# Optimization experiments

Measured on AMD Instinct MI355X. Metric: run time of the kernel, lower is better.

Reference implementation:

```python
import jax, jax.numpy as jnp
import numpy as np

B, L, IN, H, E = 64, 255, 32, 256, 128
PAD = (L - 1) // 2
DN = ('NCH', 'OIH', 'NCH')


def setup_inputs() -> dict:
    ks = jax.random.split(jax.random.key(0), 10)
    r = lambda k, shp, s=0.05: jax.random.normal(k, shp, dtype=jnp.float32) * s
    return {
        's': jax.random.normal(ks[0], (B, L, IN), dtype=jnp.float32),
        'conv1_w': r(ks[1], (H, IN, L)),
        'conv1_b': r(ks[2], (H,)),
        'bn_gamma': jnp.ones((H,), jnp.float32),
        'bn_beta': jnp.zeros((H,), jnp.float32),
        'conv2_w': r(ks[3], (E, H, L)),
        'conv2_b': r(ks[4], (E,)),
        'pw1': r(ks[5], (E, H, L)),   # stacked Linear(L, H) weights, one per channel
        'pb1': r(ks[6], (E, H)),
        'pw2': r(ks[7], (E, 2, H)),   # stacked Linear(H, 2) weights
        'pb2': r(ks[8], (E, 2)),
    }


def reference(s, conv1_w, conv1_b, bn_gamma, bn_beta, conv2_w, conv2_b, pw1, pb1, pw2, pb2):
    x = jnp.transpose(s, (0, 2, 1))  # (B, IN, T)
    h = jax.lax.conv_general_dilated(x, conv1_w, (1,), [(PAD, PAD)], dimension_numbers=DN)
    h = jax.nn.relu(h + conv1_b[None, :, None])
    # BatchNorm1d in training mode: biased batch stats over (N, T)
    mean = h.mean(axis=(0, 2), keepdims=True)
    var = ((h - mean) ** 2).mean(axis=(0, 2), keepdims=True)
    h = (h - mean) * jax.lax.rsqrt(var + 1e-5) * bn_gamma[None, :, None] + bn_beta[None, :, None]
    z = jax.lax.conv_general_dilated(h, conv2_w, (1,), [(PAD, PAD)], dimension_numbers=DN)
    z = jnp.transpose(z + conv2_b[None, :, None], (0, 2, 1))  # (B, T, E)

    rf = jnp.fft.rfft(z, axis=1)                 # (B, F, E), F = L//2 + 1 == E
    power = jnp.abs(rf)[:, :, 1:] ** 2           # faithful channel-axis slice -> (B, F, E-1)
    freq_bins = jnp.fft.rfftfreq(L)[1:]          # (F-1,) == (E-1,)
    frequency = jnp.sum(freq_bins * power, axis=1) / jnp.sum(power, axis=1)  # (B, E-1)
    amplitude = 2.0 * jnp.sqrt(jnp.sum(power, axis=1)) / L                    # (B, E-1)
    offset = rf.real[:, :, 0] / L                                              # (B, E)

    # batched per-channel 2-layer MLP (replaces Python loop over embedding_dim)
    hmid = jax.nn.relu(jnp.einsum('btc,cht->bch', z, pw1) + pb1[None])  # (B, E, H)
    ang = jnp.einsum('bch,coh->bco', hmid, pw2) + pb2[None]             # (B, E, 2)
    phase = jnp.arctan2(ang[:, :, 1], ang[:, :, 0])                     # (B, E)
    return (amplitude, phase, frequency, offset)
```

## Files before the change

kernel.cpp:

```cpp
#include <hip/hip_runtime.h>
#include <math.h>

#define TB   64
#define TT   255
#define TIN  32
#define NH   256
#define NE   128
#define NK   255
#define NPAD 127

#define NF    384
#define NBINS 193
#define NFC   386
#define FCP   416
#define W2ROW 12288
#define HSROW 16384

typedef __attribute__((ext_vector_type(8))) short short8;
typedef __attribute__((ext_vector_type(4))) float float4v;

#define WSB_W2S  0u
#define WSB_Z    0u
#define WSB_HFU  8388608u
#define WSB_HMID 8388608u
#define WSB_ZSP  18972672u
#define WSB_HS   31621120u
#define WSB_BDH  56918144u
#define WSB_BDL  57115776u
#define WSB_BDM  57313408u
#define WSB_BWH  57511040u
#define WSB_BWL  57708672u
#define WSB_BWM  57906304u
#define WSB_D1   58103936u
#define WSB_BN   58105984u

#define O_AMP   0u
#define O_PHASE 8128u
#define O_FREQ  16320u
#define O_OFF   24448u

static __device__ __forceinline__ unsigned short f2bf(float f) {
  unsigned int u = __float_as_uint(f);
  unsigned int r = (u + 0x7FFFu + ((u >> 16) & 1u)) >> 16;
  return (unsigned short)r;
}
static __device__ __forceinline__ float bf2f(unsigned short s) {
  return __uint_as_float(((unsigned int)s) << 16);
}
static __device__ __forceinline__ short8 as_s8(uint4 v) {
  union { uint4 u; short8 s; } c; c.u = v; return c.s;
}

static __device__ __forceinline__ void split3(float x, unsigned short& h,
                                              unsigned short& l, unsigned short& m2) {
  h = f2bf(x);
  float r1 = x - bf2f(h);
  l = f2bf(r1);
  m2 = f2bf(r1 - bf2f(l));
}
static __device__ __forceinline__ void split_pack2(float x0, float x1,
    unsigned int& ph, unsigned int& pl, unsigned int& pm) {
  unsigned short h0, l0, m0_, h1, l1, m1_;
  split3(x0, h0, l0, m0_);
  split3(x1, h1, l1, m1_);
  ph = (unsigned int)h0 | ((unsigned int)h1 << 16);
  pl = (unsigned int)l0 | ((unsigned int)l1 << 16);
  pm = (unsigned int)m0_ | ((unsigned int)m1_ << 16);
}

static __device__ __forceinline__ void put_hi(unsigned int* __restrict__ U, int r,
                                              int p, unsigned int v) {
  const int sw = r & 7;
  U[r * 32 + ((((p >> 2) ^ sw) << 2) | (p & 3))] = v;
}
static __device__ __forceinline__ void put_lo(unsigned int* __restrict__ U, int r,
                                              int p, unsigned int v) {
  const int sw = r & 7;
  U[r * 32 + (((((p >> 2) + 4) ^ sw) << 2) | (p & 3))] = v;
}
static __device__ __forceinline__ void stage8_3(unsigned int* __restrict__ U,
                                                unsigned int* __restrict__ U2, int r,
                                                int p0, const float* __restrict__ v) {
#pragma unroll
  for (int q = 0; q < 4; ++q) {
    unsigned int ph, pl, pm;
    split_pack2(v[2 * q], v[2 * q + 1], ph, pl, pm);
    put_hi(U, r, p0 + q, ph);
    put_lo(U, r, p0 + q, pl);
    put_hi(U2, r, p0 + q, pm);
  }
}
static __device__ __forceinline__ void stage2_3(unsigned int* __restrict__ U,
                                                unsigned int* __restrict__ U2, int r,
                                                int p, float x0, float x1) {
  unsigned int ph, pl, pm;
  split_pack2(x0, x1, ph, pl, pm);
  put_hi(U, r, p, ph);
  put_lo(U, r, p, pl);
  put_hi(U2, r, p, pm);
}
static __device__ __forceinline__ short8 frag(const unsigned short* __restrict__ lds,
                                              int row, int quad, int part) {
  return *(const short8*)&lds[row * 64 + (((quad ^ (part << 2)) ^ (row & 7)) << 3)];
}
#define MF(a, b, c) __builtin_amdgcn_mfma_f32_16x16x32_bf16((a), (b), (c), 0, 0, 0)
#define MF6(accv, ahv, alv, a2v, bhv, blv, b2v) do {                              \
    accv = MF(ahv, bhv, accv);                                                    \
    accv = MF(ahv, blv, accv);                                                    \
    accv = MF(alv, bhv, accv);                                                    \
    accv = MF(alv, blv, accv);                                                    \
    accv = MF(ahv, b2v, accv);                                                    \
    accv = MF(a2v, bhv, accv);                                                    \
  } while (0)
#define MF5(accv, ahv, alv, a2v, bhv, blv) do {                                   \
    accv = MF(ahv, bhv, accv);                                                    \
    accv = MF(ahv, blv, accv);                                                    \
    accv = MF(alv, bhv, accv);                                                    \
    accv = MF(alv, blv, accv);                                                    \
    accv = MF(a2v, bhv, accv);                                                    \
  } while (0)

__global__ __launch_bounds__(256) void init_k(
    const float* __restrict__ w1, unsigned int* __restrict__ wp1u,
    unsigned int* __restrict__ bdh, unsigned int* __restrict__ bdl,
    unsigned int* __restrict__ bdm, unsigned int* __restrict__ bwh,
    unsigned int* __restrict__ bwl, unsigned int* __restrict__ bwm,
    float* __restrict__ d1, float* __restrict__ bn) {
  __shared__ float tile[512][33];
  const int bid = blockIdx.x, tid = threadIdx.x;
  if (bid == 0) {
    bn[tid] = 0.f;
    bn[256 + tid] = 0.f;
    return;
  }
  if (bid < 387) {
    float* sv = (float*)tile;
    const int m = bid - 1, t = tid;
    const int f = m >> 1, im = m & 1;
    const float C = 6.28318530717958647692f / 384.f;
    int r1 = (f * t) % 384;
    float th1 = C * (float)r1;
    sv[t] = (t == 255) ? 0.f : (im ? -sinf(th1) : cosf(th1));
    int a = f * (t - 127);
    int r2 = a % 384; if (r2 < 0) r2 += 384;
    float th2 = C * (float)r2;
    sv[256 + t] = (t == 255) ? 0.f : (im ? sinf(th2) : cosf(th2));
    __syncthreads();
    const int which = t >> 7, j = t & 127;
    unsigned int ph, pl, pm;
    split_pack2(sv[which * 256 + 2 * j], sv[which * 256 + 2 * j + 1], ph, pl, pm);
    size_t off = (size_t)m * 128 + j;
    if (which == 0) { bdh[off] = ph; bdl[off] = pl; bdm[off] = pm; }
    else            { bwh[off] = ph; bwl[off] = pl; bwm[off] = pm; }
    return;
  }
  if (bid < 389) {
    const int fc = (bid - 387) * 256 + tid;
    if (fc >= NFC) return;
    const int f = fc >> 1, im = fc & 1;
    const float C = 6.28318530717958647692f / 384.f;
    float s = 0.f;
    int r = 0;
    for (int t = 0; t < TT; ++t) {
      float th = C * (float)r;
      s += im ? -sinf(th) : cosf(th);
      r += f; if (r >= 384) r -= 384;
    }
    d1[fc] = s;
    return;
  }
  {
    const int q = bid - 389;
    const int et = q >> 3, kc = q & 7;
    const int kk0 = kc * 32, cnt = min(32, NK - kk0);
    for (int idx = tid; idx < 512 * 32; idx += 256) {
      int row = idx >> 5, kl = idx & 31;
      if (kl < cnt) {
        int e_l = row >> 5, i_l = row & 31;
        tile[row][kl] = w1[(size_t)((et * 16 + e_l) * TIN + i_l) * NK + kk0 + kl];
      }
    }
    __syncthreads();
    const int lane = tid >> 2, jp = (tid & 3) * 2;
    const int row0 = (lane & 15) * 32 + (lane >> 4) * 8 + jp;
    for (int kl = 0; kl < cnt; ++kl) {
      float w0 = tile[row0][kl], w1v = tile[row0 + 1][kl];
      unsigned short h0 = f2bf(w0), h1 = f2bf(w1v);
      unsigned short l0 = f2bf(w0 - bf2f(h0)), l1 = f2bf(w1v - bf2f(h1));
      size_t base = (size_t)(kk0 + kl) * 8192 + et * 512 + tid;
      wp1u[base] = (unsigned int)h0 | ((unsigned int)h1 << 16);
      wp1u[base + 256] = (unsigned int)l0 | ((unsigned int)l1 << 16);
    }
  }
}

#define C1_ROWS 384
__global__ __launch_bounds__(256, 2) void conv1_mfma(
    const float* __restrict__ s, const unsigned int* __restrict__ wp1u,
    const float* __restrict__ b1v, unsigned int* __restrict__ hfu,
    float* __restrict__ bn) {
  __shared__ __align__(16) unsigned short Alds[C1_ROWS * 64];
  const int th = blockIdx.x & 1, chg = blockIdx.x >> 1, b = blockIdx.y;
  const int tid = threadIdx.x, lane = tid & 63, wv = tid >> 6;
  const int quad = lane >> 4, l15 = lane & 15;
  const int tg = wv & 1, eg = wv >> 1;
  unsigned int* Au = (unsigned int*)Alds;

  for (int idx = tid; idx < C1_ROWS * 16; idx += 256) {
    int r = idx >> 4, p = idx & 15;
    int t = th * 128 + r - NPAD;
    float v0 = 0.f, v1 = 0.f;
    if (t >= 0 && t < TT) {
      const float* sp = &s[(size_t)(b * TT + t) * TIN + p * 2];
      v0 = sp[0]; v1 = sp[1];
    }
    unsigned short h0 = f2bf(v0), h1 = f2bf(v1);
    unsigned short l0 = f2bf(v0 - bf2f(h0)), l1 = f2bf(v1 - bf2f(h1));
    int sw = r & 7;
    Au[r * 32 + ((((p >> 2) ^ sw) << 2) | (p & 3))] = (unsigned int)h0 | ((unsigned int)h1 << 16);
    Au[r * 32 + (((((p >> 2) + 4) ^ sw) << 2) | (p & 3))] = (unsigned int)l0 | ((unsigned int)l1 << 16);
  }

#define LOADB1(buf, KK) do {                                                      \
    const uint4* _b = (const uint4*)(wp1u + (size_t)(KK) * 8192u) +               \
                      (chg * 4 + eg * 2) * 128;                                   \
    buf[0] = _b[lane];          buf[1] = _b[64 + lane];                           \
    buf[2] = _b[128 + lane];    buf[3] = _b[192 + lane];                          \
  } while (0)

#define MSTEP1(KK, buf) do {                                                      \
    short8 bh0 = as_s8(buf[0]), bl0 = as_s8(buf[1]);                              \
    short8 bh1 = as_s8(buf[2]), bl1 = as_s8(buf[3]);                              \
    _Pragma("unroll")                                                             \
    for (int mi = 0; mi < 4; ++mi) {                                              \
      const int row = tg * 64 + mi * 16 + l15 + (KK);                             \
      const int sw = row & 7;                                                     \
      short8 ah = *(const short8*)&Alds[row * 64 + ((quad ^ sw) << 3)];           \
      short8 al = *(const short8*)&Alds[row * 64 + (((quad ^ 4) ^ sw) << 3)];     \
      acc[mi][0] = MF(ah, bh0, acc[mi][0]);                                       \
      acc[mi][0] = MF(ah, bl0, acc[mi][0]);                                       \
      acc[mi][0] = MF(al, bh0, acc[mi][0]);                                       \
      acc[mi][1] = MF(ah, bh1, acc[mi][1]);                                       \
      acc[mi][1] = MF(ah, bl1, acc[mi][1]);                                       \
      acc[mi][1] = MF(al, bh1, acc[mi][1]);                                       \
    }                                                                             \
  } while (0)

  uint4 b0[4], b1x[4], b2x[4];
  LOADB1(b0, 0);
  LOADB1(b1x, 1);
  LOADB1(b2x, 2);
  __syncthreads();

  float4v acc[4][2];
#pragma unroll
  for (int mi = 0; mi < 4; ++mi)
#pragma unroll
    for (int ni = 0; ni < 2; ++ni) acc[mi][ni] = (float4v)(0.f);

  for (int kp = 0; kp < 84; ++kp) {
    const int kk = kp * 3;
    MSTEP1(kk, b0);     LOADB1(b0, kk + 3);
    MSTEP1(kk + 1, b1x); LOADB1(b1x, kk + 4);
    MSTEP1(kk + 2, b2x); LOADB1(b2x, kk + 5);
  }
  MSTEP1(252, b0);
  MSTEP1(253, b1x);
  MSTEP1(254, b2x);

  float s1[2] = {0.f, 0.f}, s2[2] = {0.f, 0.f};
#pragma unroll
  for (int mi = 0; mi < 4; ++mi) {
#pragma unroll
    for (int ni = 0; ni < 2; ++ni) {
      int ch = chg * 64 + (eg * 2 + ni) * 16 + l15;
      float bias = b1v[ch];
#pragma unroll
      for (int r = 0; r < 4; ++r) {
        int t = th * 128 + tg * 64 + mi * 16 + quad * 4 + r;
        if (t < TT) {
          float v = fmaxf(acc[mi][ni][r] + bias, 0.f);
          unsigned short vh = f2bf(v);
          unsigned short vl = f2bf(v - bf2f(vh));
          hfu[(size_t)(b * 256 + t) * NH + ch] =
              (unsigned int)vh | ((unsigned int)vl << 16);
          s1[ni] += v; s2[ni] += v * v;
        }
      }
    }
  }
#pragma unroll
  for (int ni = 0; ni < 2; ++ni) {
    s1[ni] += __shfl_xor(s1[ni], 16);
    s1[ni] += __shfl_xor(s1[ni], 32);
    s2[ni] += __shfl_xor(s2[ni], 16);
    s2[ni] += __shfl_xor(s2[ni], 32);
    if (quad == 0) {
      int ch = chg * 64 + (eg * 2 + ni) * 16 + l15;
      atomicAdd(&bn[ch], s1[ni]);
      atomicAdd(&bn[256 + ch], s2[ni]);
    }
  }
#undef LOADB1
#undef MSTEP1
}


#define LOAD_A_PLANES(PH, PL, PM) do {                                            \
    if (fcA < NFC) {                                                              \
      size_t ab = (size_t)fcA * 128 + (k0 >> 1) + hfA * 8;                        \
      uint4 h0v = *(const uint4*)(PH + ab), h1v = *(const uint4*)(PH + ab + 4);   \
      uint4 l0v = *(const uint4*)(PL + ab), l1v = *(const uint4*)(PL + ab + 4);   \
      uint4 m0v = *(const uint4*)(PM + ab), m1v = *(const uint4*)(PM + ab + 4);   \
      _Pragma("unroll")                                                           \
      for (int q = 0; q < 4; ++q) {                                               \
        put_hi(Au, rA, hfA * 8 + q, ((const unsigned int*)&h0v)[q]);              \
        put_hi(Au, rA, hfA * 8 + 4 + q, ((const unsigned int*)&h1v)[q]);          \
        put_lo(Au, rA, hfA * 8 + q, ((const unsigned int*)&l0v)[q]);              \
        put_lo(Au, rA, hfA * 8 + 4 + q, ((const unsigned int*)&l1v)[q]);          \
        put_hi(A2u, rA, hfA * 8 + q, ((const unsigned int*)&m0v)[q]);             \
        put_hi(A2u, rA, hfA * 8 + 4 + q, ((const unsigned int*)&m1v)[q]);         \
      }                                                                           \
    } else {                                                                      \
      _Pragma("unroll")                                                           \
      for (int q = 0; q < 8; ++q) {                                               \
        put_hi(Au, rA, hfA * 8 + q, 0u);                                          \
        put_lo(Au, rA, hfA * 8 + q, 0u);                                          \
        put_hi(A2u, rA, hfA * 8 + q, 0u);                                         \
      }                                                                           \
    }                                                                             \
  } while (0)

__global__ __launch_bounds__(256, 2) void dftH_mfma(
    const unsigned int* __restrict__ hfu, const float* __restrict__ bn,
    const float* __restrict__ gamma, const float* __restrict__ beta,
    const unsigned int* __restrict__ bdh, const unsigned int* __restrict__ bdl,
    const unsigned int* __restrict__ bdm, const float* __restrict__ d1,
    float* __restrict__ H) {
  __shared__ __align__(16) unsigned short Alds[128 * 64];
  __shared__ __align__(16) unsigned short A2lds[128 * 64];
  __shared__ __align__(16) unsigned short Blds[64 * 64];
  __shared__ float scs[64], shs[64];
  const int b = blockIdx.x, m0 = blockIdx.y * 128, h0c = blockIdx.z * 64;
  const int tid = threadIdx.x, lane = tid & 63, wv = tid >> 6;
  const int quad = lane >> 4, l15 = lane & 15;
  const int wm = wv >> 1, wn = wv & 1;
  const int hl = tid & 63, g = tid >> 6;
  unsigned int* Au = (unsigned int*)Alds;
  unsigned int* A2u = (unsigned int*)A2lds;
  unsigned int* Bu = (unsigned int*)Blds;

  if (tid < 64) {
    int h = h0c + tid;
    const float inv = 1.0f / (TB * TT);
    float m = bn[h] * inv;
    float var = bn[256 + h] * inv - m * m;
    float sc = gamma[h] / sqrtf(var + 1e-5f);
    scs[tid] = sc;
    shs[tid] = beta[h] - m * sc;
  }

  float4v acc[4][2];
#pragma unroll
  for (int i = 0; i < 4; ++i)
#pragma unroll
    for (int j = 0; j < 2; ++j) acc[i][j] = (float4v)(0.f);

  const int rA = tid >> 1, hfA = tid & 1;
  const int fcA = m0 + rA;

  for (int kk = 0; kk < 8; ++kk) {
    const int k0 = kk * 32;
    if (kk) __syncthreads();
    LOAD_A_PLANES(bdh, bdl, bdm);
#pragma unroll
    for (int j = 0; j < 4; ++j) {
      int tp = g * 4 + j;
      int t0 = k0 + tp * 2;
      unsigned int u0 = (t0 < TT)
          ? hfu[(size_t)(b * 256 + t0) * NH + h0c + hl] : 0u;
      unsigned int u1 = (t0 + 1 < TT)
          ? hfu[(size_t)(b * 256 + t0 + 1) * NH + h0c + hl] : 0u;
      unsigned int hp = (u0 & 0xFFFFu) | ((u1 & 0xFFFFu) << 16);
      unsigned int lp = (u0 >> 16) | (u1 & 0xFFFF0000u);
      put_hi(Bu, hl, tp, hp);
      put_lo(Bu, hl, tp, lp);
    }
    __syncthreads();
    short8 bh[2], bl[2];
#pragma unroll
    for (int ni = 0; ni < 2; ++ni) {
      int rb = wn * 32 + ni * 16 + l15;
      bh[ni] = frag(Blds, rb, quad, 0);
      bl[ni] = frag(Blds, rb, quad, 1);
    }
#pragma unroll
    for (int mi = 0; mi < 4; ++mi) {
      int ra = wm * 64 + mi * 16 + l15;
      short8 ah = frag(Alds, ra, quad, 0);
      short8 al = frag(Alds, ra, quad, 1);
      short8 a2 = frag(A2lds, ra, quad, 0);
#pragma unroll
      for (int ni = 0; ni < 2; ++ni) MF5(acc[mi][ni], ah, al, a2, bh[ni], bl[ni]);
    }
  }
#pragma unroll
  for (int mi = 0; mi < 4; ++mi) {
    int fc0 = m0 + wm * 64 + mi * 16 + quad * 4;
#pragma unroll
    for (int ni = 0; ni < 2; ++ni) {
      int hli = wn * 32 + ni * 16 + l15;
      float scv = scs[hli];
      float shv = shs[hli];
#pragma unroll
      for (int r = 0; r < 4; ++r) {
        int fc = fc0 + r;
        if (fc < NFC)
          H[(size_t)fc * HSROW + b * 256 + h0c + hli] =
              scv * acc[mi][ni][r] + shv * d1[fc];
      }
    }
  }
}

__global__ __launch_bounds__(256, 2) void w2prep_mfma(
    const float* __restrict__ w2, const unsigned int* __restrict__ bwh,
    const unsigned int* __restrict__ bwl, const unsigned int* __restrict__ bwm,
    float* __restrict__ W, int h0c, int hcnt) {
  __shared__ __align__(16) unsigned short Alds[128 * 64];
  __shared__ __align__(16) unsigned short A2lds[128 * 64];
  __shared__ __align__(16) unsigned short Blds[128 * 64];
  __shared__ __align__(16) unsigned short B2lds[128 * 64];
  const int n0 = blockIdx.x * 128, m0 = blockIdx.y * 128;
  const int tid = threadIdx.x, lane = tid & 63, wv = tid >> 6;
  const int quad = lane >> 4, l15 = lane & 15;
  const int wm = wv >> 1, wn = wv & 1;
  unsigned int* Au = (unsigned int*)Alds;
  unsigned int* A2u = (unsigned int*)A2lds;
  unsigned int* Bu = (unsigned int*)Blds;
  unsigned int* B2u = (unsigned int*)B2lds;

  float4v acc[4][4];
#pragma unroll
  for (int i = 0; i < 4; ++i)
#pragma unroll
    for (int j = 0; j < 4; ++j) acc[i][j] = (float4v)(0.f);

  const int rA = tid >> 1, hfA = tid & 1;
  const int fcA = m0 + rA;
  const int lane8 = tid & 7, rsub = tid >> 3;

  for (int kk = 0; kk < 8; ++kk) {
    const int k0 = kk * 32;
    if (kk) __syncthreads();
    LOAD_A_PLANES(bwh, bwl, bwm);
#pragma unroll
    for (int pass = 0; pass < 4; ++pass) {
      int row = pass * 32 + rsub;
      int n = n0 + row;
      int e = n / 96, hl = n - e * 96;
      int ok = (hl < hcnt);
      const float* src = w2 + ((size_t)(e * NH + h0c + hl)) * NK;
      int kb = k0 + lane8 * 4;
      float f0 = (ok && kb < NK) ? src[kb] : 0.f;
      float f1 = (ok && kb + 1 < NK) ? src[kb + 1] : 0.f;
      float f2 = (ok && kb + 2 < NK) ? src[kb + 2] : 0.f;
      float f3 = (ok && kb + 3 < NK) ? src[kb + 3] : 0.f;
      stage2_3(Bu, B2u, row, lane8 * 2, f0, f1);
      stage2_3(Bu, B2u, row, lane8 * 2 + 1, f2, f3);
    }
    __syncthreads();
    short8 bh[4], bl[4], b2[4];
#pragma unroll
    for (int ni = 0; ni < 4; ++ni) {
      int rb = wn * 64 + ni * 16 + l15;
      bh[ni] = frag(Blds, rb, quad, 0);
      bl[ni] = frag(Blds, rb, quad, 1);
      b2[ni] = frag(B2lds, rb, quad, 0);
    }
#pragma unroll
    for (int mi = 0; mi < 4; ++mi) {
      int ra = wm * 64 + mi * 16 + l15;
      short8 ah = frag(Alds, ra, quad, 0);
      short8 al = frag(Alds, ra, quad, 1);
      short8 a2 = frag(A2lds, ra, quad, 0);
#pragma unroll
      for (int ni = 0; ni < 4; ++ni) MF6(acc[mi][ni], ah, al, a2, bh[ni], bl[ni], b2[ni]);
    }
  }
#pragma unroll
  for (int mi = 0; mi < 4; ++mi) {
    int fc0 = m0 + wm * 64 + mi * 16 + quad * 4;
#pragma unroll
    for (int ni = 0; ni < 4; ++ni) {
      int n = n0 + wn * 64 + ni * 16 + l15;
#pragma unroll
      for (int r = 0; r < 4; ++r) {
        if (fc0 + r < NFC) W[(size_t)(fc0 + r) * W2ROW + n] = acc[mi][ni][r];
      }
    }
  }
}

__global__ __launch_bounds__(256, 2) void fgemm_mfma(
    const float* __restrict__ H, const float* __restrict__ W,
    float* __restrict__ zsp, int c96, int nks, int first) {
  __shared__ __align__(16) unsigned short Alds[64 * 64];
  __shared__ __align__(16) unsigned short A2lds[64 * 64];
  __shared__ __align__(16) unsigned short Blds[128 * 64];
  __shared__ __align__(16) unsigned short B2lds[128 * 64];
  const int ri = blockIdx.x, f = blockIdx.y;
  const int tid = threadIdx.x, lane = tid & 63, wv = tid >> 6;
  const int quad = lane >> 4, l15 = lane & 15;
  const int wm = wv >> 1, wn = wv & 1;
  unsigned int* Au = (unsigned int*)Alds;
  unsigned int* A2u = (unsigned int*)A2lds;
  unsigned int* Bu = (unsigned int*)Blds;
  unsigned int* B2u = (unsigned int*)B2lds;

  float4v acc[2][4];
#pragma unroll
  for (int i = 0; i < 2; ++i)
#pragma unroll
    for (int j = 0; j < 4; ++j) acc[i][j] = (float4v)(0.f);

  const int rA = tid >> 2, qA = tid & 3;
  const int rB = tid >> 1, hB = tid & 1;

  for (int ph = 0; ph < 2 * nks; ++ph) {
    const int ca = (ph >= nks) ? 1 : 0;
    const int hsub = (ph - ca * nks) * 32;
    if (ph) __syncthreads();
    {
      float va[8];
      const float4* s4 = (const float4*)(H + (size_t)(2 * f + ca) * HSROW +
                                         rA * 256 + c96 + hsub + qA * 8);
      *(float4*)(va + 0) = s4[0]; *(float4*)(va + 4) = s4[1];
      stage8_3(Au, A2u, rA, qA * 4, va);
    }
    {
      const int cb = ri ^ ca;
      const int neg = (ri == 0 && ca == 1);
      float vb[16];
      const float4* s4 = (const float4*)(W + (size_t)(2 * f + cb) * W2ROW +
                                         rB * 96 + hsub + hB * 16);
      *(float4*)(vb + 0) = s4[0]; *(float4*)(vb + 4) = s4[1];
      *(float4*)(vb + 8) = s4[2]; *(float4*)(vb + 12) = s4[3];
      if (neg) {
#pragma unroll
        for (int q = 0; q < 16; ++q) vb[q] = -vb[q];
      }
      stage8_3(Bu, B2u, rB, hB * 8, vb);
      stage8_3(Bu, B2u, rB, hB * 8 + 4, vb + 8);
    }
    __syncthreads();
    short8 bh[4], bl[4], b2[4];
#pragma unroll
    for (int ni = 0; ni < 4; ++ni) {
      int rb = wn * 64 + ni * 16 + l15;
      bh[ni] = frag(Blds, rb, quad, 0);
      bl[ni] = frag(Blds, rb, quad, 1);
      b2[ni] = frag(B2lds, rb, quad, 0);
    }
#pragma unroll
    for (int mi = 0; mi < 2; ++mi) {
      int ra = wm * 32 + mi * 16 + l15;
      short8 ah = frag(Alds, ra, quad, 0);
      short8 al = frag(Alds, ra, quad, 1);
      short8 a2 = frag(A2lds, ra, quad, 0);
#pragma unroll
      for (int ni = 0; ni < 4; ++ni) MF6(acc[mi][ni], ah, al, a2, bh[ni], bl[ni], b2[ni]);
    }
  }
  float* Z = zsp + (size_t)(2 * f + ri) * 8192;
#pragma unroll
  for (int mi = 0; mi < 2; ++mi) {
#pragma unroll
    for (int ni = 0; ni < 4; ++ni) {
      int e = wn * 64 + ni * 16 + l15;
#pragma unroll
      for (int r = 0; r < 4; ++r) {
        int b = wm * 32 + mi * 16 + quad * 4 + r;
        size_t off = (size_t)b * 128 + e;
        if (first) Z[off] = acc[mi][ni][r];
        else       Z[off] += acc[mi][ni][r];
      }
    }
  }
}

__global__ __launch_bounds__(256, 2) void idft_mfma(
    const float* __restrict__ zsp, const unsigned int* __restrict__ bdh,
    const unsigned int* __restrict__ bdl, const unsigned int* __restrict__ bdm,
    const float* __restrict__ b2, float* __restrict__ z) {
  __shared__ __align__(16) unsigned short Alds[128 * 64];
  __shared__ __align__(16) unsigned short A2lds[128 * 64];
  __shared__ __align__(16) unsigned short Blds[64 * 64];
  __shared__ __align__(16) unsigned short B2lds[64 * 64];
  const int n0 = blockIdx.x * 64, m0 = blockIdx.y * 128;
  const int tid = threadIdx.x, lane = tid & 63, wv = tid >> 6;
  const int quad = lane >> 4, l15 = lane & 15;
  const int wm = wv >> 1, wn = wv & 1;
  const int tl = tid & 63, g = tid >> 6;
  unsigned int* Au = (unsigned int*)Alds;
  unsigned int* A2u = (unsigned int*)A2lds;
  unsigned int* Bu = (unsigned int*)Blds;
  unsigned int* B2u = (unsigned int*)B2lds;

  float4v acc[4][2];
#pragma unroll
  for (int i = 0; i < 4; ++i)
#pragma unroll
    for (int j = 0; j < 2; ++j) acc[i][j] = (float4v)(0.f);

  for (int kk = 0; kk < 13; ++kk) {
    const int k0 = kk * 32;
    if (kk) __syncthreads();
#pragma unroll
    for (int i = 0; i < 8; ++i) {
      int combo = i * 4 + g;
      int tp = combo >> 1, beh = combo & 1;
      int fc0 = k0 + tp * 2;
      int row = beh * 64 + lane;
      float v0 = (fc0 < NFC) ? zsp[(size_t)fc0 * 8192 + m0 + row] : 0.f;
      float v1 = (fc0 + 1 < NFC) ? zsp[(size_t)(fc0 + 1) * 8192 + m0 + row] : 0.f;
      stage2_3(Au, A2u, row, tp, v0, v1);
    }
#pragma unroll
    for (int j = 0; j < 4; ++j) {
      int tp = g * 4 + j;
      int fc0 = k0 + tp * 2;
      float x0 = 0.f, x1 = 0.f;
      if (fc0 < NFC) {
        int fq = fc0 >> 1;
        float sw = ((fq == 0 || fq == 192) ? 1.f : 2.f) * (1.f / 384.f);
        int t = n0 + tl;
        int pi = t >> 1, hs = (t & 1) * 16;
        size_t o0 = (size_t)fc0 * 128 + pi, o1 = o0 + 128;
        x0 = (bf2f((unsigned short)(bdh[o0] >> hs)) +
              bf2f((unsigned short)(bdl[o0] >> hs)) +
              bf2f((unsigned short)(bdm[o0] >> hs))) * sw;
        x1 = (bf2f((unsigned short)(bdh[o1] >> hs)) +
              bf2f((unsigned short)(bdl[o1] >> hs)) +
              bf2f((unsigned short)(bdm[o1] >> hs))) * sw;
      }
      stage2_3(Bu, B2u, tl, tp, x0, x1);
    }
    __syncthreads();
    short8 bh[2], bl[2], b2f[2];
#pragma unroll
    for (int ni = 0; ni < 2; ++ni) {
      int rb = wn * 32 + ni * 16 + l15;
      bh[ni] = frag(Blds, rb, quad, 0);
      bl[ni] = frag(Blds, rb, quad, 1);
      b2f[ni] = frag(B2lds, rb, quad, 0);
    }
#pragma unroll
    for (int mi = 0; mi < 4; ++mi) {
      int ra = wm * 64 + mi * 16 + l15;
      short8 ah = frag(Alds, ra, quad, 0);
      short8 al = frag(Alds, ra, quad, 1);
      short8 a2 = frag(A2lds, ra, quad, 0);
#pragma unroll
      for (int ni = 0; ni < 2; ++ni) MF6(acc[mi][ni], ah, al, a2, bh[ni], bl[ni], b2f[ni]);
    }
  }
#pragma unroll
  for (int mi = 0; mi < 4; ++mi) {
#pragma unroll
    for (int ni = 0; ni < 2; ++ni) {
      int t = n0 + wn * 32 + ni * 16 + l15;
#pragma unroll
      for (int r = 0; r < 4; ++r) {
        int be = m0 + wm * 64 + mi * 16 + quad * 4 + r;
        if (t < TT) z[(size_t)be * TT + t] = acc[mi][ni][r] + b2[be & 127];
      }
    }
  }
}

__global__ __launch_bounds__(256) void mlp1_k(const float* __restrict__ z,
                                              const float* __restrict__ pw1,
                                              const float* __restrict__ pb1,
                                              float* __restrict__ hmid) {
  const int TC = 128;
  __shared__ float zl[TC * 68];
  __shared__ float pl[TC * 68];
  const int c = blockIdx.y, h0 = blockIdx.x * 64, tid = threadIdx.x;
  const int h4 = tid & 15, b4 = tid >> 4;
  float acc[4][4];
#pragma unroll
  for (int a = 0; a < 4; ++a)
#pragma unroll
    for (int bb = 0; bb < 4; ++bb) acc[a][bb] = 0.f;
  for (int t0 = 0; t0 < TT; t0 += TC) {
    const int tc = min(TC, TT - t0);
    __syncthreads();
    for (int idx = tid; idx < 64 * tc; idx += 256) {
      int r = idx / tc, t = idx - r * tc;
      zl[t * 68 + r] = z[(size_t)(r * NE + c) * TT + t0 + t];
      pl[t * 68 + r] = pw1[(size_t)(c * NH + h0 + r) * TT + t0 + t];
    }
    __syncthreads();
    for (int t = 0; t < tc; ++t) {
      float4 zv = *(const float4*)&zl[t * 68 + b4 * 4];
      float4 pv = *(const float4*)&pl[t * 68 + h4 * 4];
      float zz[4] = {zv.x, zv.y, zv.z, zv.w};
      float pp[4] = {pv.x, pv.y, pv.z, pv.w};
#pragma unroll
      for (int a = 0; a < 4; ++a)
#pragma unroll
        for (int bb = 0; bb < 4; ++bb) acc[a][bb] = fmaf(pp[a], zz[bb], acc[a][bb]);
    }
  }
#pragma unroll
  for (int a = 0; a < 4; ++a) {
    int hh = h0 + h4 * 4 + a;
    float bias = pb1[c * NH + hh];
#pragma unroll
    for (int bb = 0; bb < 4; ++bb) {
      int bidx = b4 * 4 + bb;
      float v = acc[a][bb] + bias;
      hmid[(size_t)(bidx * NE + c) * NH + hh] = fmaxf(v, 0.f);
    }
  }
}

__global__ __launch_bounds__(256) void tail_k(const float* __restrict__ hmid,
                                              const float* __restrict__ pw2,
                                              const float* __restrict__ pb2,
                                              const float* __restrict__ z,
                                              float* __restrict__ out) {
  __shared__ float zr[TT];
  __shared__ float ct[TT];
  const int bid = blockIdx.x, tid = threadIdx.x;
  const int lane = tid & 63, wv = tid >> 6;
  if (bid < 2048) {
    const int p = bid * 4 + wv;
    const int b = p >> 7, c = p & 127;
    const float4 hv = *(const float4*)&hmid[(size_t)(b * NE + c) * NH + lane * 4];
    const float4 p0 = *(const float4*)&pw2[(size_t)(c * 2 + 0) * NH + lane * 4];
    const float4 p1 = *(const float4*)&pw2[(size_t)(c * 2 + 1) * NH + lane * 4];
    float s0 = hv.x * p0.x + hv.y * p0.y + hv.z * p0.z + hv.w * p0.w;
    float s1 = hv.x * p1.x + hv.y * p1.y + hv.z * p1.z + hv.w * p1.w;
#pragma unroll
    for (int off = 32; off; off >>= 1) {
      s0 += __shfl_down(s0, off);
      s1 += __shfl_down(s1, off);
    }
    if (lane == 0) {
      float a0 = s0 + pb2[c * 2 + 0];
      float a1 = s1 + pb2[c * 2 + 1];
      out[O_PHASE + b * NE + c] = atan2f(a1, a0);
    }
    return;
  }
  if (bid < 4096) {
    const int q = bid - 2048;
    const int b = q >> 5, c = (q & 31) * 4 + wv;
    const float* row = z + (size_t)(b * NE + c) * TT;
    float s1 = 0.f, s2 = 0.f;
    for (int idx = lane; idx < TT; idx += 64) {
      float v = row[idx];
      s1 += v; s2 += v * v;
    }
#pragma unroll
    for (int off = 32; off; off >>= 1) {
      s1 += __shfl_down(s1, off);
      s2 += __shfl_down(s2, off);
    }
    if (lane == 0 && c >= 1) {
      float P = 0.5f * (255.f * s2 + s1 * s1);
      out[O_AMP + b * 127 + (c - 1)] = 2.f * sqrtf(P) / 255.f;
      out[O_FREQ + b * 127 + (c - 1)] = (float)c / 255.f;
    }
    return;
  }
  {
    const int b = bid - 4096;
    for (int idx = tid; idx < TT; idx += 256) {
      zr[idx] = z[(size_t)(b * NE + 0) * TT + idx];
      ct[idx] = cosf(6.283185307179586f * (float)idx / 255.f);
    }
    __syncthreads();
    if (tid < 128) {
      const int f = tid;
      float s = 0.f;
      int m = 0;
      for (int t = 0; t < TT; ++t) {
        s += zr[t] * ct[m];
        m += f; if (m >= TT) m -= TT;
      }
      out[O_OFF + b * NE + f] = s / 255.f;
    }
  }
}

extern "C" void kernel_launch(void* const* d_in, const int* in_sizes, int n_in,
                              void* d_out, int out_size, void* d_ws, size_t ws_size,
                              hipStream_t stream) {
  (void)in_sizes; (void)n_in; (void)out_size; (void)ws_size;
  const float* s       = (const float*)d_in[0];
  const float* conv1_w = (const float*)d_in[1];
  const float* conv1_b = (const float*)d_in[2];
  const float* bn_g    = (const float*)d_in[3];
  const float* bn_b    = (const float*)d_in[4];
  const float* conv2_w = (const float*)d_in[5];
  const float* conv2_b = (const float*)d_in[6];
  const float* pw1     = (const float*)d_in[7];
  const float* pb1     = (const float*)d_in[8];
  const float* pw2     = (const float*)d_in[9];
  const float* pb2     = (const float*)d_in[10];
  float* out = (float*)d_out;
  char* ws   = (char*)d_ws;

  unsigned int* wp1u = (unsigned int*)(ws + WSB_W2S);
  float* z    = (float*)(ws + WSB_Z);
  unsigned int* hfu = (unsigned int*)(ws + WSB_HFU);
  float* hmid = (float*)(ws + WSB_HMID);
  float* W2s  = (float*)(ws + WSB_W2S);
  float* Hs   = (float*)(ws + WSB_HS);
  float* zsp  = (float*)(ws + WSB_ZSP);
  unsigned int* bdh = (unsigned int*)(ws + WSB_BDH);
  unsigned int* bdl = (unsigned int*)(ws + WSB_BDL);
  unsigned int* bdm = (unsigned int*)(ws + WSB_BDM);
  unsigned int* bwh = (unsigned int*)(ws + WSB_BWH);
  unsigned int* bwl = (unsigned int*)(ws + WSB_BWL);
  unsigned int* bwm = (unsigned int*)(ws + WSB_BWM);
  float* d1 = (float*)(ws + WSB_D1);
  float* bn = (float*)(ws + WSB_BN);

  init_k<<<517, 256, 0, stream>>>(conv1_w, wp1u, bdh, bdl, bdm, bwh, bwl, bwm, d1, bn);
  conv1_mfma<<<dim3(8, TB), 256, 0, stream>>>(s, wp1u, conv1_b, hfu, bn);
  dftH_mfma<<<dim3(64, 4, 4), 256, 0, stream>>>(hfu, bn, bn_g, bn_b,
                                                bdh, bdl, bdm, d1, Hs);
  const int h0cs[3] = {0, 96, 192};
  const int hcnts[3] = {96, 96, 64};
  const int nkss[3] = {3, 3, 2};
  for (int c = 0; c < 3; ++c) {
    w2prep_mfma<<<dim3(96, 4), 256, 0, stream>>>(conv2_w, bwh, bwl, bwm, W2s,
                                                 h0cs[c], hcnts[c]);
    fgemm_mfma<<<dim3(2, NBINS), 256, 0, stream>>>(Hs, W2s, zsp,
                                                   h0cs[c], nkss[c], c == 0 ? 1 : 0);
  }
  idft_mfma<<<dim3(4, 64), 256, 0, stream>>>(zsp, bdh, bdl, bdm, conv2_b, z);
  mlp1_k<<<dim3(4, NE), 256, 0, stream>>>(z, pw1, pb1, hmid);
  tail_k<<<4160, 256, 0, stream>>>(hmid, pw2, pb2, z, out);
}
```

Baseline: 628.3 us.

## Compute conv1 via frequency-domain DFT GEMMs instead of direct MFMA convolution

Replaces the direct time-domain conv1 MFMA kernel (with bf16 hi/lo weight prepacking) with a spectral pipeline. Input and conv1 weights are transformed by DFT GEMMs, multiplied per frequency bin as complex GEMMs, then inverse-transformed with bias, ReLU and BN statistic accumulation fused in. This mirrors the approach already used for conv2 and cuts the O(L) per-output tap work. In exchange it adds two extra kernel launches, larger fp32 intermediates in workspace, and 3-way bf16 split arithmetic whose accuracy may differ from the previous 2-way split.

```diff
diff --git a/kernel.cpp b/kernel.cpp
--- a/kernel.cpp
+++ b/kernel.cpp
@@ -12,18 +12,20 @@
 #define NF    384
 #define NBINS 193
 #define NFC   386
-#define FCP   416
 #define W2ROW 12288
 #define HSROW 16384
 
 typedef __attribute__((ext_vector_type(8))) short short8;
 typedef __attribute__((ext_vector_type(4))) float float4v;
 
+#define WSB_SSP  0u
 #define WSB_W2S  0u
 #define WSB_Z    0u
+#define WSB_W1SP 4194304u
 #define WSB_HFU  8388608u
 #define WSB_HMID 8388608u
 #define WSB_ZSP  18972672u
+#define WSB_C1SP 25165824u
 #define WSB_HS   31621120u
 #define WSB_BDH  56918144u
 #define WSB_BDL  57115776u
@@ -46,9 +48,6 @@
 }
 static __device__ __forceinline__ float bf2f(unsigned short s) {
   return __uint_as_float(((unsigned int)s) << 16);
-}
-static __device__ __forceinline__ short8 as_s8(uint4 v) {
-  union { uint4 u; short8 s; } c; c.u = v; return c.s;
 }
 
 static __device__ __forceinline__ void split3(float x, unsigned short& h,
@@ -119,192 +118,6 @@
     accv = MF(alv, blv, accv);                                                    \
     accv = MF(a2v, bhv, accv);                                                    \
   } while (0)
-
-__global__ __launch_bounds__(256) void init_k(
-    const float* __restrict__ w1, unsigned int* __restrict__ wp1u,
-    unsigned int* __restrict__ bdh, unsigned int* __restrict__ bdl,
-    unsigned int* __restrict__ bdm, unsigned int* __restrict__ bwh,
-    unsigned int* __restrict__ bwl, unsigned int* __restrict__ bwm,
-    float* __restrict__ d1, float* __restrict__ bn) {
-  __shared__ float tile[512][33];
-  const int bid = blockIdx.x, tid = threadIdx.x;
-  if (bid == 0) {
-    bn[tid] = 0.f;
-    bn[256 + tid] = 0.f;
-    return;
-  }
-  if (bid < 387) {
-    float* sv = (float*)tile;
-    const int m = bid - 1, t = tid;
-    const int f = m >> 1, im = m & 1;
-    const float C = 6.28318530717958647692f / 384.f;
-    int r1 = (f * t) % 384;
-    float th1 = C * (float)r1;
-    sv[t] = (t == 255) ? 0.f : (im ? -sinf(th1) : cosf(th1));
-    int a = f * (t - 127);
-    int r2 = a % 384; if (r2 < 0) r2 += 384;
-    float th2 = C * (float)r2;
-    sv[256 + t] = (t == 255) ? 0.f : (im ? sinf(th2) : cosf(th2));
-    __syncthreads();
-    const int which = t >> 7, j = t & 127;
-    unsigned int ph, pl, pm;
-    split_pack2(sv[which * 256 + 2 * j], sv[which * 256 + 2 * j + 1], ph, pl, pm);
-    size_t off = (size_t)m * 128 + j;
-    if (which == 0) { bdh[off] = ph; bdl[off] = pl; bdm[off] = pm; }
-    else            { bwh[off] = ph; bwl[off] = pl; bwm[off] = pm; }
-    return;
-  }
-  if (bid < 389) {
-    const int fc = (bid - 387) * 256 + tid;
-    if (fc >= NFC) return;
-    const int f = fc >> 1, im = fc & 1;
-    const float C = 6.28318530717958647692f / 384.f;
-    float s = 0.f;
-    int r = 0;
-    for (int t = 0; t < TT; ++t) {
-      float th = C * (float)r;
-      s += im ? -sinf(th) : cosf(th);
-      r += f; if (r >= 384) r -= 384;
-    }
-    d1[fc] = s;
-    return;
-  }
-  {
-    const int q = bid - 389;
-    const int et = q >> 3, kc = q & 7;
-    const int kk0 = kc * 32, cnt = min(32, NK - kk0);
-    for (int idx = tid; idx < 512 * 32; idx += 256) {
-      int row = idx >> 5, kl = idx & 31;
-      if (kl < cnt) {
-        int e_l = row >> 5, i_l = row & 31;
-        tile[row][kl] = w1[(size_t)((et * 16 + e_l) * TIN + i_l) * NK + kk0 + kl];
-      }
-    }
-    __syncthreads();
-    const int lane = tid >> 2, jp = (tid & 3) * 2;
-    const int row0 = (lane & 15) * 32 + (lane >> 4) * 8 + jp;
-    for (int kl = 0; kl < cnt; ++kl) {
-      float w0 = tile[row0][kl], w1v = tile[row0 + 1][kl];
-      unsigned short h0 = f2bf(w0), h1 = f2bf(w1v);
-      unsigned short l0 = f2bf(w0 - bf2f(h0)), l1 = f2bf(w1v - bf2f(h1));
-      size_t base = (size_t)(kk0 + kl) * 8192 + et * 512 + tid;
-      wp1u[base] = (unsigned int)h0 | ((unsigned int)h1 << 16);
-      wp1u[base + 256] = (unsigned int)l0 | ((unsigned int)l1 << 16);
-    }
-  }
-}
-
-#define C1_ROWS 384
-__global__ __launch_bounds__(256, 2) void conv1_mfma(
-    const float* __restrict__ s, const unsigned int* __restrict__ wp1u,
-    const float* __restrict__ b1v, unsigned int* __restrict__ hfu,
-    float* __restrict__ bn) {
-  __shared__ __align__(16) unsigned short Alds[C1_ROWS * 64];
-  const int th = blockIdx.x & 1, chg = blockIdx.x >> 1, b = blockIdx.y;
-  const int tid = threadIdx.x, lane = tid & 63, wv = tid >> 6;
-  const int quad = lane >> 4, l15 = lane & 15;
-  const int tg = wv & 1, eg = wv >> 1;
-  unsigned int* Au = (unsigned int*)Alds;
-
-  for (int idx = tid; idx < C1_ROWS * 16; idx += 256) {
-    int r = idx >> 4, p = idx & 15;
-    int t = th * 128 + r - NPAD;
-    float v0 = 0.f, v1 = 0.f;
-    if (t >= 0 && t < TT) {
-      const float* sp = &s[(size_t)(b * TT + t) * TIN + p * 2];
-      v0 = sp[0]; v1 = sp[1];
-    }
-    unsigned short h0 = f2bf(v0), h1 = f2bf(v1);
-    unsigned short l0 = f2bf(v0 - bf2f(h0)), l1 = f2bf(v1 - bf2f(h1));
-    int sw = r & 7;
-    Au[r * 32 + ((((p >> 2) ^ sw) << 2) | (p & 3))] = (unsigned int)h0 | ((unsigned int)h1 << 16);
-    Au[r * 32 + (((((p >> 2) + 4) ^ sw) << 2) | (p & 3))] = (unsigned int)l0 | ((unsigned int)l1 << 16);
-  }
-
-#define LOADB1(buf, KK) do {                                                      \
-    const uint4* _b = (const uint4*)(wp1u + (size_t)(KK) * 8192u) +               \
-                      (chg * 4 + eg * 2) * 128;                                   \
-    buf[0] = _b[lane];          buf[1] = _b[64 + lane];                           \
-    buf[2] = _b[128 + lane];    buf[3] = _b[192 + lane];                          \
-  } while (0)
-
-#define MSTEP1(KK, buf) do {                                                      \
-    short8 bh0 = as_s8(buf[0]), bl0 = as_s8(buf[1]);                              \
-    short8 bh1 = as_s8(buf[2]), bl1 = as_s8(buf[3]);                              \
-    _Pragma("unroll")                                                             \
-    for (int mi = 0; mi < 4; ++mi) {                                              \
-      const int row = tg * 64 + mi * 16 + l15 + (KK);                             \
-      const int sw = row & 7;                                                     \
-      short8 ah = *(const short8*)&Alds[row * 64 + ((quad ^ sw) << 3)];           \
-      short8 al = *(const short8*)&Alds[row * 64 + (((quad ^ 4) ^ sw) << 3)];     \
-      acc[mi][0] = MF(ah, bh0, acc[mi][0]);                                       \
-      acc[mi][0] = MF(ah, bl0, acc[mi][0]);                                       \
-      acc[mi][0] = MF(al, bh0, acc[mi][0]);                                       \
-      acc[mi][1] = MF(ah, bh1, acc[mi][1]);                                       \
-      acc[mi][1] = MF(ah, bl1, acc[mi][1]);                                       \
-      acc[mi][1] = MF(al, bh1, acc[mi][1]);                                       \
-    }                                                                             \
-  } while (0)
-
-  uint4 b0[4], b1x[4], b2x[4];
-  LOADB1(b0, 0);
-  LOADB1(b1x, 1);
-  LOADB1(b2x, 2);
-  __syncthreads();
-
-  float4v acc[4][2];
-#pragma unroll
-  for (int mi = 0; mi < 4; ++mi)
-#pragma unroll
-    for (int ni = 0; ni < 2; ++ni) acc[mi][ni] = (float4v)(0.f);
-
-  for (int kp = 0; kp < 84; ++kp) {
-    const int kk = kp * 3;
-    MSTEP1(kk, b0);     LOADB1(b0, kk + 3);
-    MSTEP1(kk + 1, b1x); LOADB1(b1x, kk + 4);
-    MSTEP1(kk + 2, b2x); LOADB1(b2x, kk + 5);
-  }
-  MSTEP1(252, b0);
-  MSTEP1(253, b1x);
-  MSTEP1(254, b2x);
-
-  float s1[2] = {0.f, 0.f}, s2[2] = {0.f, 0.f};
-#pragma unroll
-  for (int mi = 0; mi < 4; ++mi) {
-#pragma unroll
-    for (int ni = 0; ni < 2; ++ni) {
-      int ch = chg * 64 + (eg * 2 + ni) * 16 + l15;
-      float bias = b1v[ch];
-#pragma unroll
-      for (int r = 0; r < 4; ++r) {
-        int t = th * 128 + tg * 64 + mi * 16 + quad * 4 + r;
-        if (t < TT) {
-          float v = fmaxf(acc[mi][ni][r] + bias, 0.f);
-          unsigned short vh = f2bf(v);
-          unsigned short vl = f2bf(v - bf2f(vh));
-          hfu[(size_t)(b * 256 + t) * NH + ch] =
-              (unsigned int)vh | ((unsigned int)vl << 16);
-          s1[ni] += v; s2[ni] += v * v;
-        }
-      }
-    }
-  }
-#pragma unroll
-  for (int ni = 0; ni < 2; ++ni) {
-    s1[ni] += __shfl_xor(s1[ni], 16);
-    s1[ni] += __shfl_xor(s1[ni], 32);
-    s2[ni] += __shfl_xor(s2[ni], 16);
-    s2[ni] += __shfl_xor(s2[ni], 32);
-    if (quad == 0) {
-      int ch = chg * 64 + (eg * 2 + ni) * 16 + l15;
-      atomicAdd(&bn[ch], s1[ni]);
-      atomicAdd(&bn[256 + ch], s2[ni]);
-    }
-  }
-#undef LOADB1
-#undef MSTEP1
-}
-
 
 #define LOAD_A_PLANES(PH, PL, PM) do {                                            \
     if (fcA < NFC) {                                                              \
@@ -331,6 +144,359 @@
     }                                                                             \
   } while (0)
 
+__global__ __launch_bounds__(256) void init_k(
+    unsigned int* __restrict__ bdh, unsigned int* __restrict__ bdl,
+    unsigned int* __restrict__ bdm, unsigned int* __restrict__ bwh,
+    unsigned int* __restrict__ bwl, unsigned int* __restrict__ bwm,
+    float* __restrict__ d1, float* __restrict__ bn) {
+  __shared__ float sv[512];
+  const int bid = blockIdx.x, tid = threadIdx.x;
+  if (bid == 0) {
+    bn[tid] = 0.f;
+    bn[256 + tid] = 0.f;
+    return;
+  }
+  if (bid < 387) {
+    const int m = bid - 1, t = tid;
+    const int f = m >> 1, im = m & 1;
+    const float C = 6.28318530717958647692f / 384.f;
+    int r1 = (f * t) % 384;
+    float th1 = C * (float)r1;
+    sv[t] = (t == 255) ? 0.f : (im ? -sinf(th1) : cosf(th1));
+    int a = f * (t - 127);
+    int r2 = a % 384; if (r2 < 0) r2 += 384;
+    float th2 = C * (float)r2;
+    sv[256 + t] = (t == 255) ? 0.f : (im ? sinf(th2) : cosf(th2));
+    __syncthreads();
+    const int which = t >> 7, j = t & 127;
+    unsigned int ph, pl, pm;
+    split_pack2(sv[which * 256 + 2 * j], sv[which * 256 + 2 * j + 1], ph, pl, pm);
+    size_t off = (size_t)m * 128 + j;
+    if (which == 0) { bdh[off] = ph; bdl[off] = pl; bdm[off] = pm; }
+    else            { bwh[off] = ph; bwl[off] = pl; bwm[off] = pm; }
+    return;
+  }
+  {
+    const int fc = (bid - 387) * 256 + tid;
+    if (fc >= NFC) return;
+    const int f = fc >> 1, im = fc & 1;
+    const float C = 6.28318530717958647692f / 384.f;
+    float s = 0.f;
+    int r = 0;
+    for (int t = 0; t < TT; ++t) {
+      float th = C * (float)r;
+      s += im ? -sinf(th) : cosf(th);
+      r += f; if (r >= 384) r -= 384;
+    }
+    d1[fc] = s;
+  }
+}
+
+__global__ __launch_bounds__(256, 2) void spw1_k(
+    const float* __restrict__ s, const float* __restrict__ w1,
+    const unsigned int* __restrict__ bdh, const unsigned int* __restrict__ bdl,
+    const unsigned int* __restrict__ bdm, const unsigned int* __restrict__ bwh,
+    const unsigned int* __restrict__ bwl, const unsigned int* __restrict__ bwm,
+    float* __restrict__ Ssp, float* __restrict__ W1sp) {
+  __shared__ __align__(16) unsigned short Alds[128 * 64];
+  __shared__ __align__(16) unsigned short A2lds[128 * 64];
+  __shared__ __align__(16) unsigned short Blds[128 * 64];
+  __shared__ __align__(16) unsigned short B2lds[128 * 64];
+  const int bid = blockIdx.x;
+  const int role = (bid < 64) ? 0 : 1;
+  const int bx = role ? (bid - 64) : bid;
+  const int n0 = role ? (bx & 63) * 128 : (bx & 15) * 128;
+  const int m0 = role ? (bx >> 6) * 128 : (bx >> 4) * 128;
+  const int tid = threadIdx.x, lane = tid & 63, wv = tid >> 6;
+  const int quad = lane >> 4, l15 = lane & 15;
+  const int wm = wv >> 1, wn = wv & 1;
+  unsigned int* Au = (unsigned int*)Alds;
+  unsigned int* A2u = (unsigned int*)A2lds;
+  unsigned int* Bu = (unsigned int*)Blds;
+  unsigned int* B2u = (unsigned int*)B2lds;
+  const unsigned int* PH = role ? bwh : bdh;
+  const unsigned int* PL = role ? bwl : bdl;
+  const unsigned int* PM = role ? bwm : bdm;
+
+  float4v acc[4][4];
+#pragma unroll
+  for (int i = 0; i < 4; ++i)
+#pragma unroll
+    for (int j = 0; j < 4; ++j) acc[i][j] = (float4v)(0.f);
+
+  const int rA = tid >> 1, hfA = tid & 1;
+  const int fcA = m0 + rA;
+  const int lane8 = tid & 7, rsub = tid >> 3;
+
+  for (int kk = 0; kk < 8; ++kk) {
+    const int k0 = kk * 32;
+    if (kk) __syncthreads();
+    LOAD_A_PLANES(PH, PL, PM);
+    if (role == 0) {
+      int n = n0 + rA;
+      int bI = n >> 5, ii = n & 31;
+      float vb[16];
+#pragma unroll
+      for (int q = 0; q < 16; ++q) {
+        int t = k0 + hfA * 16 + q;
+        vb[q] = (t < TT) ? s[((size_t)bI * TT + t) * TIN + ii] : 0.f;
+      }
+      stage8_3(Bu, B2u, rA, hfA * 8, vb);
+      stage8_3(Bu, B2u, rA, hfA * 8 + 4, vb + 8);
+    } else {
+#pragma unroll
+      for (int pass = 0; pass < 4; ++pass) {
+        int row = pass * 32 + rsub;
+        const float* src = w1 + (size_t)(n0 + row) * NK;
+        int kb = k0 + lane8 * 4;
+        float f0 = (kb < NK) ? src[kb] : 0.f;
+        float f1 = (kb + 1 < NK) ? src[kb + 1] : 0.f;
+        float f2 = (kb + 2 < NK) ? src[kb + 2] : 0.f;
+        float f3 = (kb + 3 < NK) ? src[kb + 3] : 0.f;
+        stage2_3(Bu, B2u, row, lane8 * 2, f0, f1);
+        stage2_3(Bu, B2u, row, lane8 * 2 + 1, f2, f3);
+      }
+    }
+    __syncthreads();
+    short8 bh[4], bl[4], b2[4];
+#pragma unroll
+    for (int ni = 0; ni < 4; ++ni) {
+      int rb = wn * 64 + ni * 16 + l15;
+      bh[ni] = frag(Blds, rb, quad, 0);
+      bl[ni] = frag(Blds, rb, quad, 1);
+      b2[ni] = frag(B2lds, rb, quad, 0);
+    }
+#pragma unroll
+    for (int mi = 0; mi < 4; ++mi) {
+      int ra = wm * 64 + mi * 16 + l15;
+      short8 ah = frag(Alds, ra, quad, 0);
+      short8 al = frag(Alds, ra, quad, 1);
+      short8 a2 = frag(A2lds, ra, quad, 0);
+#pragma unroll
+      for (int ni = 0; ni < 4; ++ni) MF6(acc[mi][ni], ah, al, a2, bh[ni], bl[ni], b2[ni]);
+    }
+  }
+  float* outp = role ? W1sp : Ssp;
+  const int NN = role ? 8192 : 2048;
+#pragma unroll
+  for (int mi = 0; mi < 4; ++mi) {
+    int fc0 = m0 + wm * 64 + mi * 16 + quad * 4;
+#pragma unroll
+    for (int ni = 0; ni < 4; ++ni) {
+      int n = n0 + wn * 64 + ni * 16 + l15;
+#pragma unroll
+      for (int r = 0; r < 4; ++r) {
+        if (fc0 + r < NFC) outp[(size_t)(fc0 + r) * NN + n] = acc[mi][ni][r];
+      }
+    }
+  }
+}
+
+__global__ __launch_bounds__(256, 2) void fgemm1_k(
+    const float* __restrict__ Ssp, const float* __restrict__ W1sp,
+    float* __restrict__ C1sp) {
+  __shared__ __align__(16) unsigned short Alds[64 * 64];
+  __shared__ __align__(16) unsigned short A2lds[64 * 64];
+  __shared__ __align__(16) unsigned short Blds[128 * 64];
+  __shared__ __align__(16) unsigned short B2lds[128 * 64];
+  const int ri = blockIdx.x & 1, n0 = (blockIdx.x >> 1) * 128;
+  const int f = blockIdx.y;
+  const int tid = threadIdx.x, lane = tid & 63, wv = tid >> 6;
+  const int quad = lane >> 4, l15 = lane & 15;
+  const int wm = wv >> 1, wn = wv & 1;
+  unsigned int* Au = (unsigned int*)Alds;
+  unsigned int* A2u = (unsigned int*)A2lds;
+  unsigned int* Bu = (unsigned int*)Blds;
+  unsigned int* B2u = (unsigned int*)B2lds;
+
+  float4v acc[2][4];
+#pragma unroll
+  for (int i = 0; i < 2; ++i)
+#pragma unroll
+    for (int j = 0; j < 4; ++j) acc[i][j] = (float4v)(0.f);
+
+  const int rA = tid >> 2, qA = tid & 3;
+  const int rB = tid >> 1, hB = tid & 1;
+
+  for (int ph = 0; ph < 2; ++ph) {
+    const int ca = ph;
+    if (ph) __syncthreads();
+    {
+      float va[8];
+      const float4* s4 = (const float4*)(Ssp + (size_t)(2 * f + ca) * 2048 +
+                                         rA * 32 + qA * 8);
+      *(float4*)(va + 0) = s4[0]; *(float4*)(va + 4) = s4[1];
+      stage8_3(Au, A2u, rA, qA * 4, va);
+    }
+    {
+      const int cb = ri ^ ca;
+      const int neg = (ri == 0 && ca == 1);
+      float vb[16];
+      const float4* s4 = (const float4*)(W1sp + (size_t)(2 * f + cb) * 8192 +
+                                         (n0 + rB) * 32 + hB * 16);
+      *(float4*)(vb + 0) = s4[0]; *(float4*)(vb + 4) = s4[1];
+      *(float4*)(vb + 8) = s4[2]; *(float4*)(vb + 12) = s4[3];
+      if (neg) {
+#pragma unroll
+        for (int q = 0; q < 16; ++q) vb[q] = -vb[q];
+      }
+      stage8_3(Bu, B2u, rB, hB * 8, vb);
+      stage8_3(Bu, B2u, rB, hB * 8 + 4, vb + 8);
+    }
+    __syncthreads();
+    short8 bh[4], bl[4], b2[4];
+#pragma unroll
+    for (int ni = 0; ni < 4; ++ni) {
+      int rb = wn * 64 + ni * 16 + l15;
+      bh[ni] = frag(Blds, rb, quad, 0);
+      bl[ni] = frag(Blds, rb, quad, 1);
+      b2[ni] = frag(B2lds, rb, quad, 0);
+    }
+#pragma unroll
+    for (int mi = 0; mi < 2; ++mi) {
+      int ra = wm * 32 + mi * 16 + l15;
+      short8 ah = frag(Alds, ra, quad, 0);
+      short8 al = frag(Alds, ra, quad, 1);
+      short8 a2 = frag(A2lds, ra, quad, 0);
+#pragma unroll
+      for (int ni = 0; ni < 4; ++ni) MF6(acc[mi][ni], ah, al, a2, bh[ni], bl[ni], b2[ni]);
+    }
+  }
+  float* Z = C1sp + (size_t)(2 * f + ri) * 16384;
+#pragma unroll
+  for (int mi = 0; mi < 2; ++mi) {
+#pragma unroll
+    for (int ni = 0; ni < 4; ++ni) {
+      int h = n0 + wn * 64 + ni * 16 + l15;
+#pragma unroll
+      for (int r = 0; r < 4; ++r) {
+        int b = wm * 32 + mi * 16 + quad * 4 + r;
+        Z[(size_t)b * 256 + h] = acc[mi][ni][r];
+      }
+    }
+  }
+}
+
+__global__ __launch_bounds__(256, 2) void idft1_k(
+    const float* __restrict__ C1sp, const unsigned int* __restrict__ bdh,
+    const unsigned int* __restrict__ bdl, const unsigned int* __restrict__ bdm,
+    const float* __restrict__ b1v, unsigned int* __restrict__ hfu,
+    float* __restrict__ bn) {
+  __shared__ __align__(16) unsigned short Alds[128 * 64];
+  __shared__ __align__(16) unsigned short A2lds[128 * 64];
+  __shared__ __align__(16) unsigned short Blds[128 * 64];
+  __shared__ __align__(16) unsigned short B2lds[128 * 64];
+  const int n0 = (blockIdx.x & 1) * 128;
+  const int m0 = (blockIdx.x >> 1) * 128;
+  const int b = blockIdx.y;
+  const int tid = threadIdx.x, lane = tid & 63, wv = tid >> 6;
+  const int quad = lane >> 4, l15 = lane & 15;
+  const int wm = wv >> 1, wn = wv & 1;
+  unsigned int* Au = (unsigned int*)Alds;
+  unsigned int* A2u = (unsigned int*)A2lds;
+  unsigned int* Bu = (unsigned int*)Blds;
+  unsigned int* B2u = (unsigned int*)B2lds;
+
+  float4v acc[4][4];
+#pragma unroll
+  for (int i = 0; i < 4; ++i)
+#pragma unroll
+    for (int j = 0; j < 4; ++j) acc[i][j] = (float4v)(0.f);
+
+  const int rA = tid >> 1, hfA = tid & 1;
+  const int chq = tid & 127, half = tid >> 7;
+
+  for (int kk = 0; kk < 13; ++kk) {
+    const int k0 = kk * 32;
+    if (kk) __syncthreads();
+    {
+      int t = m0 + rA;
+      int pi = t >> 1, hs = (t & 1) * 16;
+#pragma unroll
+      for (int q = 0; q < 8; ++q) {
+        int p = hfA * 8 + q;
+        int fc0 = k0 + 2 * p;
+        float x0 = 0.f, x1 = 0.f;
+        if (fc0 < NFC) {
+          int fq = fc0 >> 1;
+          float sw = ((fq == 0 || fq == 192) ? 1.f : 2.f) * (1.f / 384.f);
+          size_t o0 = (size_t)fc0 * 128 + pi, o1 = o0 + 128;
+          x0 = (bf2f((unsigned short)(bdh[o0] >> hs)) +
+                bf2f((unsigned short)(bdl[o0] >> hs)) +
+                bf2f((unsigned short)(bdm[o0] >> hs))) * sw;
+          x1 = (bf2f((unsigned short)(bdh[o1] >> hs)) +
+                bf2f((unsigned short)(bdl[o1] >> hs)) +
+                bf2f((unsigned short)(bdm[o1] >> hs))) * sw;
+        }
+        stage2_3(Au, A2u, rA, p, x0, x1);
+      }
+    }
+    {
+#pragma unroll
+      for (int q = 0; q < 8; ++q) {
+        int p = half * 8 + q;
+        int fc0 = k0 + 2 * p;
+        float v0 = (fc0 < NFC)
+            ? C1sp[(size_t)fc0 * 16384 + b * 256 + n0 + chq] : 0.f;
+        float v1 = (fc0 + 1 < NFC)
+            ? C1sp[(size_t)(fc0 + 1) * 16384 + b * 256 + n0 + chq] : 0.f;
+        stage2_3(Bu, B2u, chq, p, v0, v1);
+      }
+    }
+    __syncthreads();
+    short8 bh[4], bl[4], b2[4];
+#pragma unroll
+    for (int ni = 0; ni < 4; ++ni) {
+      int rb = wn * 64 + ni * 16 + l15;
+      bh[ni] = frag(Blds, rb, quad, 0);
+      bl[ni] = frag(Blds, rb, quad, 1);
+      b2[ni] = frag(B2lds, rb, quad, 0);
+    }
+#pragma unroll
+    for (int mi = 0; mi < 4; ++mi) {
+      int ra = wm * 64 + mi * 16 + l15;
+      short8 ah = frag(Alds, ra, quad, 0);
+      short8 al = frag(Alds, ra, quad, 1);
+      short8 a2 = frag(A2lds, ra, quad, 0);
+#pragma unroll
+      for (int ni = 0; ni < 4; ++ni) MF6(acc[mi][ni], ah, al, a2, bh[ni], bl[ni], b2[ni]);
+    }
+  }
+  float s1[4] = {0.f, 0.f, 0.f, 0.f}, s2[4] = {0.f, 0.f, 0.f, 0.f};
+#pragma unroll
+  for (int ni = 0; ni < 4; ++ni) {
+    int ch = n0 + wn * 64 + ni * 16 + l15;
+    float bias = b1v[ch];
+#pragma unroll
+    for (int mi = 0; mi < 4; ++mi) {
+#pragma unroll
+      for (int r = 0; r < 4; ++r) {
+        int t = m0 + wm * 64 + mi * 16 + quad * 4 + r;
+        if (t < TT) {
+          float v = fmaxf(acc[mi][ni][r] + bias, 0.f);
+          unsigned short vh = f2bf(v);
+          unsigned short vl = f2bf(v - bf2f(vh));
+          hfu[(size_t)(b * 256 + t) * NH + ch] =
+              (unsigned int)vh | ((unsigned int)vl << 16);
+          s1[ni] += v; s2[ni] += v * v;
+        }
+      }
+    }
+  }
+#pragma unroll
+  for (int ni = 0; ni < 4; ++ni) {
+    s1[ni] += __shfl_xor(s1[ni], 16);
+    s1[ni] += __shfl_xor(s1[ni], 32);
+    s2[ni] += __shfl_xor(s2[ni], 16);
+    s2[ni] += __shfl_xor(s2[ni], 32);
+    if (quad == 0) {
+      int ch = n0 + wn * 64 + ni * 16 + l15;
+      atomicAdd(&bn[ch], s1[ni]);
+      atomicAdd(&bn[256 + ch], s2[ni]);
+    }
+  }
+}
+
 __global__ __launch_bounds__(256, 2) void dftH_mfma(
     const unsigned int* __restrict__ hfu, const float* __restrict__ bn,
     const float* __restrict__ gamma, const float* __restrict__ beta,
@@ -814,7 +980,9 @@
   float* out = (float*)d_out;
   char* ws   = (char*)d_ws;
 
-  unsigned int* wp1u = (unsigned int*)(ws + WSB_W2S);
+  float* Ssp  = (float*)(ws + WSB_SSP);
+  float* W1sp = (float*)(ws + WSB_W1SP);
+  float* C1sp = (float*)(ws + WSB_C1SP);
   float* z    = (float*)(ws + WSB_Z);
   unsigned int* hfu = (unsigned int*)(ws + WSB_HFU);
   float* hmid = (float*)(ws + WSB_HMID);
@@ -830,8 +998,11 @@
   float* d1 = (float*)(ws + WSB_D1);
   float* bn = (float*)(ws + WSB_BN);
 
-  init_k<<<517, 256, 0, stream>>>(conv1_w, wp1u, bdh, bdl, bdm, bwh, bwl, bwm, d1, bn);
-  conv1_mfma<<<dim3(8, TB), 256, 0, stream>>>(s, wp1u, conv1_b, hfu, bn);
+  init_k<<<389, 256, 0, stream>>>(bdh, bdl, bdm, bwh, bwl, bwm, d1, bn);
+  spw1_k<<<320, 256, 0, stream>>>(s, conv1_w, bdh, bdl, bdm, bwh, bwl, bwm,
+                                  Ssp, W1sp);
+  fgemm1_k<<<dim3(4, NBINS), 256, 0, stream>>>(Ssp, W1sp, C1sp);
+  idft1_k<<<dim3(4, TB), 256, 0, stream>>>(C1sp, bdh, bdl, bdm, conv1_b, hfu, bn);
   dftH_mfma<<<dim3(64, 4, 4), 256, 0, stream>>>(hfu, bn, bn_g, bn_b,
                                                 bdh, bdl, bdm, d1, Hs);
   const int h0cs[3] = {0, 96, 192};
```

Result: slower. 754.0 us (+20.0%).
